# Optimization experiments

Hardware: AMD Instinct MI355X
Metric: run time of the kernel (lower is better)

The kernel has to match this reference:

```python
import jax, jax.numpy as jnp
import numpy as np

KH, KW = 3, 3

def setup_inputs() -> dict:
    key = jax.random.key(0)
    kx, kw = jax.random.split(key)
    X = jax.random.normal(kx, (4096, 8192), dtype=jnp.float32)
    # nn.Parameter(torch.rand(kernel_size)) -> uniform [0,1)
    weight = jax.random.uniform(kw, (KH, KW), dtype=jnp.float32)
    bias = jnp.zeros((1,), dtype=jnp.float32)
    return {"X": X, "weight": weight, "bias": bias}

def reference(X, weight, bias):
    # valid 2D cross-correlation (lax conv does correlation, no kernel flip)
    # X: [H, W]; weight: [kh, kw] -> out: [H-kh+1, W-kw+1]
    out = jax.lax.conv_general_dilated(
        X[None, None, :, :],            # NCHW, N=C=1
        weight[None, None, :, :],        # OIHW, O=I=1
        window_strides=(1, 1),
        padding="VALID",
    )[0, 0]
    return out + bias
```

## Files before the change

### kernel.cpp

```cpp
#include <hip/hip_runtime.h>

#define H  4096
#define W  8192
#define KH 3
#define KW 3
#define HO (H - KH + 1)
#define WO (W - KW + 1)
#define CPT 4
#define RPS 4
#define SPB 4
#define BAND (RPS * SPB)
#define BLK 256

__global__ __launch_bounds__(BLK) void ConvLayer_4140348473931_kernel(
    const float* __restrict__ X, const float* __restrict__ Wt,
    const float* __restrict__ Bias, float* __restrict__ Out)
{
    const int tid   = threadIdx.x;
    const int c0    = blockIdx.x * (BLK * CPT) + tid * CPT;
    const int rbase = blockIdx.y * BAND;
    const int cext  = min(c0 + 4, W - 2);

    float w[9];
#pragma unroll
    for (int i = 0; i < 9; ++i) w[i] = Wt[i];
    const float bias = Bias[0];

    float x[RPS + 2][6];
    float pre[RPS][6];

#define LOADROW(rr, dst)                                                     \
    do {                                                                     \
        int _r = (rr); if (_r > H - 1) _r = H - 1;                           \
        const float* _row = X + (size_t)_r * W;                              \
        float4 _v  = *reinterpret_cast<const float4*>(_row + c0);            \
        float2 _v2 = *reinterpret_cast<const float2*>(_row + cext);         \
        (dst)[0] = _v.x;  (dst)[1] = _v.y;  (dst)[2] = _v.z;                 \
        (dst)[3] = _v.w;  (dst)[4] = _v2.x; (dst)[5] = _v2.y;               \
    } while (0)

#pragma unroll
    for (int ir = 0; ir < 6; ++ir) LOADROW(rbase + ir, x[ir]);

#pragma unroll
    for (int s = 0; s < SPB; ++s) {
        if (s < SPB - 1) {
#pragma unroll
            for (int ir = 0; ir < RPS; ++ir)
                LOADROW(rbase + s * RPS + 6 + ir, pre[ir]);
        }

        float acc[RPS][CPT];
#pragma unroll
        for (int i = 0; i < RPS; ++i) {
#pragma unroll
            for (int j = 0; j < CPT; ++j) {
                float ss = bias;
#pragma unroll
                for (int kh = 0; kh < KH; ++kh)
#pragma unroll
                    for (int kw = 0; kw < KW; ++kw)
                        ss = fmaf(w[kh * 3 + kw], x[i + kh][j + kw], ss);
                acc[i][j] = ss;
            }
        }

        {
            const int r0 = rbase + s * RPS;
            const bool full = (c0 + CPT <= WO);
#pragma unroll
            for (int i = 0; i < RPS; ++i) {
                int r = r0 + i;
                if (r < HO) {
                    float* orow = Out + (size_t)r * WO + c0;
                    *reinterpret_cast<float2*>(orow) = make_float2(acc[i][0], acc[i][1]);
                    if (full)
                        *reinterpret_cast<float2*>(orow + 2) = make_float2(acc[i][2], acc[i][3]);
                }
            }
        }

        if (s < SPB - 1) {
#pragma unroll
            for (int j = 0; j < 6; ++j) { x[0][j] = x[4][j]; x[1][j] = x[5][j]; }
#pragma unroll
            for (int ir = 0; ir < RPS; ++ir)
#pragma unroll
                for (int j = 0; j < 6; ++j) x[2 + ir][j] = pre[ir][j];
        }
    }
#undef LOADROW
}

extern "C" void kernel_launch(void* const* d_in, const int* in_sizes, int n_in,
                              void* d_out, int out_size, void* d_ws, size_t ws_size,
                              hipStream_t stream) {
    const float* X    = (const float*)d_in[0];
    const float* Wt   = (const float*)d_in[1];
    const float* Bias = (const float*)d_in[2];
    float* Out        = (float*)d_out;

    dim3 block(BLK);
    dim3 grid((WO + BLK * CPT - 1) / (BLK * CPT),
              (HO + BAND - 1) / BAND);
    ConvLayer_4140348473931_kernel<<<grid, block, 0, stream>>>(X, Wt, Bias, Out);
}
```

Baseline: 48.87 us.

## Double-buffer row prefetch two stages ahead and double band height

Swaps the single prefetch buffer for two alternating buffers so that loads for stage s+2 are issued while stage s is computed and stored. The band per block grows from 16 to 32 rows, which halves the redundant halo-row reads, and launch bounds now request 4 blocks per SM. The goal is more memory-level parallelism in a bandwidth-bound stencil. In exchange it uses more registers and launches half as many blocks, which lowers parallelism.

```diff
diff --git a/kernel.cpp b/kernel.cpp
--- a/kernel.cpp
+++ b/kernel.cpp
@@ -8,11 +8,11 @@
 #define WO (W - KW + 1)
 #define CPT 4
 #define RPS 4
-#define SPB 4
+#define SPB 8
 #define BAND (RPS * SPB)
 #define BLK 256
 
-__global__ __launch_bounds__(BLK) void ConvLayer_4140348473931_kernel(
+__global__ __launch_bounds__(BLK, 4) void ConvLayer_4140348473931_kernel(
     const float* __restrict__ X, const float* __restrict__ Wt,
     const float* __restrict__ Bias, float* __restrict__ Out)
 {
@@ -26,70 +26,89 @@
     for (int i = 0; i < 9; ++i) w[i] = Wt[i];
     const float bias = Bias[0];
 
-    float x[RPS + 2][6];
-    float pre[RPS][6];
+    float x[6][6];
+    float preA[4][6];
+    float preB[4][6];
 
 #define LOADROW(rr, dst)                                                     \
     do {                                                                     \
         int _r = (rr); if (_r > H - 1) _r = H - 1;                           \
         const float* _row = X + (size_t)_r * W;                              \
         float4 _v  = *reinterpret_cast<const float4*>(_row + c0);            \
-        float2 _v2 = *reinterpret_cast<const float2*>(_row + cext);         \
+        float2 _v2 = *reinterpret_cast<const float2*>(_row + cext);          \
         (dst)[0] = _v.x;  (dst)[1] = _v.y;  (dst)[2] = _v.z;                 \
-        (dst)[3] = _v.w;  (dst)[4] = _v2.x; (dst)[5] = _v2.y;               \
+        (dst)[3] = _v.w;  (dst)[4] = _v2.x; (dst)[5] = _v2.y;                \
+    } while (0)
+
+#define PREFETCH(t, buf)                                                     \
+    do {                                                                     \
+        if ((t) < SPB) {                                                     \
+            _Pragma("unroll")                                                \
+            for (int _ir = 0; _ir < RPS; ++_ir)                              \
+                LOADROW(rbase + (t) * RPS + 2 + _ir, (buf)[_ir]);            \
+        }                                                                    \
+    } while (0)
+
+#define COMPUTE_STORE(s)                                                     \
+    do {                                                                     \
+        float acc[RPS][CPT];                                                 \
+        _Pragma("unroll")                                                    \
+        for (int _i = 0; _i < RPS; ++_i) {                                   \
+            _Pragma("unroll")                                                \
+            for (int _j = 0; _j < CPT; ++_j) {                               \
+                float _s = bias;                                             \
+                _Pragma("unroll")                                            \
+                for (int _kh = 0; _kh < KH; ++_kh)                           \
+                    _Pragma("unroll")                                        \
+                    for (int _kw = 0; _kw < KW; ++_kw)                       \
+                        _s = fmaf(w[_kh * 3 + _kw], x[_i + _kh][_j + _kw], _s); \
+                acc[_i][_j] = _s;                                            \
+            }                                                                \
+        }                                                                    \
+        const int _r0 = rbase + (s) * RPS;                                   \
+        const bool _full = (c0 + CPT <= WO);                                 \
+        _Pragma("unroll")                                                    \
+        for (int _i = 0; _i < RPS; ++_i) {                                   \
+            int _r = _r0 + _i;                                               \
+            if (_r < HO) {                                                   \
+                float* _orow = Out + (size_t)_r * WO + c0;                   \
+                *reinterpret_cast<float2*>(_orow) = make_float2(acc[_i][0], acc[_i][1]); \
+                if (_full)                                                   \
+                    *reinterpret_cast<float2*>(_orow + 2) = make_float2(acc[_i][2], acc[_i][3]); \
+            }                                                                \
+        }                                                                    \
+    } while (0)
+
+#define SHIFT_FROM(buf)                                                      \
+    do {                                                                     \
+        _Pragma("unroll")                                                    \
+        for (int _j = 0; _j < 6; ++_j) { x[0][_j] = x[4][_j]; x[1][_j] = x[5][_j]; } \
+        _Pragma("unroll")                                                    \
+        for (int _ir = 0; _ir < RPS; ++_ir)                                  \
+            _Pragma("unroll")                                                \
+            for (int _j = 0; _j < 6; ++_j) x[2 + _ir][_j] = (buf)[_ir][_j];  \
     } while (0)
 
 #pragma unroll
     for (int ir = 0; ir < 6; ++ir) LOADROW(rbase + ir, x[ir]);
+    PREFETCH(1, preA);
 
 #pragma unroll
-    for (int s = 0; s < SPB; ++s) {
-        if (s < SPB - 1) {
-#pragma unroll
-            for (int ir = 0; ir < RPS; ++ir)
-                LOADROW(rbase + s * RPS + 6 + ir, pre[ir]);
-        }
+    for (int p = 0; p < SPB / 2; ++p) {
+        const int s0 = 2 * p;
+        PREFETCH(s0 + 2, preB);
+        COMPUTE_STORE(s0);
+        SHIFT_FROM(preA);
 
-        float acc[RPS][CPT];
-#pragma unroll
-        for (int i = 0; i < RPS; ++i) {
-#pragma unroll
-            for (int j = 0; j < CPT; ++j) {
-                float ss = bias;
-#pragma unroll
-                for (int kh = 0; kh < KH; ++kh)
-#pragma unroll
-                    for (int kw = 0; kw < KW; ++kw)
-                        ss = fmaf(w[kh * 3 + kw], x[i + kh][j + kw], ss);
-                acc[i][j] = ss;
-            }
-        }
+        PREFETCH(s0 + 3, preA);
+        COMPUTE_STORE(s0 + 1);
+        if (s0 + 2 < SPB) SHIFT_FROM(preB);
+    }
 
-        {
-            const int r0 = rbase + s * RPS;
-            const bool full = (c0 + CPT <= WO);
-#pragma unroll
-            for (int i = 0; i < RPS; ++i) {
-                int r = r0 + i;
-                if (r < HO) {
-                    float* orow = Out + (size_t)r * WO + c0;
-                    *reinterpret_cast<float2*>(orow) = make_float2(acc[i][0], acc[i][1]);
-                    if (full)
-                        *reinterpret_cast<float2*>(orow + 2) = make_float2(acc[i][2], acc[i][3]);
-                }
-            }
-        }
-
-        if (s < SPB - 1) {
-#pragma unroll
-            for (int j = 0; j < 6; ++j) { x[0][j] = x[4][j]; x[1][j] = x[5][j]; }
-#pragma unroll
-            for (int ir = 0; ir < RPS; ++ir)
-#pragma unroll
-                for (int j = 0; j < 6; ++j) x[2 + ir][j] = pre[ir][j];
-        }
-    }
 #undef LOADROW
+#undef PREFETCH
+#undef COMPUTE_STORE
+#undef SHIFT_FROM
 }
 
 extern "C" void kernel_launch(void* const* d_in, const int* in_sizes, int n_in,
```

New measurement: 47.56 us (median of 2 runs). -2.7%, faster.

## Stage input tiles into LDS with async global_load_lds double buffering

Applied to the files above, without the earlier changes.

Replaces the per-thread register sliding-window loads with block tiles of 18x256 floats staged into shared memory through direct global-to-LDS loads, double buffered across 8 row tiles per block. Hand-placed vmcnt waits and barriers overlap the fetch of the next tile with the compute of the current one. The aim is to remove the redundant overlapping float2 halo loads and hide memory latency. In exchange it adds barriers, LDS traffic and halo recomputation, since each 256-wide tile yields only 252 output columns and 16-row tiles re-read 2 halo rows.

```diff
diff --git a/kernel.cpp b/kernel.cpp
--- a/kernel.cpp
+++ b/kernel.cpp
@@ -1,95 +1,127 @@
 #include <hip/hip_runtime.h>
 
-#define H  4096
-#define W  8192
-#define KH 3
-#define KW 3
-#define HO (H - KH + 1)
-#define WO (W - KW + 1)
-#define CPT 4
-#define RPS 4
-#define SPB 4
-#define BAND (RPS * SPB)
+#define H   4096
+#define W   8192
+#define HO  4094
+#define WO  8190
+#define TWI 256
+#define TWO 252
+#define TH  16
+#define IH  18
+#define TPB 8
 #define BLK 256
+
+typedef __attribute__((address_space(3))) void       lds_void;
+typedef __attribute__((address_space(1))) const void glob_void;
 
 __global__ __launch_bounds__(BLK) void ConvLayer_4140348473931_kernel(
     const float* __restrict__ X, const float* __restrict__ Wt,
     const float* __restrict__ Bias, float* __restrict__ Out)
 {
-    const int tid   = threadIdx.x;
-    const int c0    = blockIdx.x * (BLK * CPT) + tid * CPT;
-    const int rbase = blockIdx.y * BAND;
-    const int cext  = min(c0 + 4, W - 2);
+    __shared__ float bufA[IH][TWI];
+    __shared__ float bufB[IH][TWI];
+
+    const int tid  = threadIdx.x;
+    const int lane = tid & 63;
+    const int wav  = tid >> 6;
+
+    const int Cbase = blockIdx.x * TWO;
+    const int Rblk  = blockIdx.y * (TPB * TH);
+
+    const int gcol = min(Cbase + 4 * lane, W - 4);
 
     float w[9];
 #pragma unroll
     for (int i = 0; i < 9; ++i) w[i] = Wt[i];
     const float bias = Bias[0];
 
-    float x[RPS + 2][6];
-    float pre[RPS][6];
+    const int lr = wav * 4;
+    const int lc = lane * 4;
+    const int oc = Cbase + lc;
 
-#define LOADROW(rr, dst)                                                     \
-    do {                                                                     \
-        int _r = (rr); if (_r > H - 1) _r = H - 1;                           \
-        const float* _row = X + (size_t)_r * W;                              \
-        float4 _v  = *reinterpret_cast<const float4*>(_row + c0);            \
-        float2 _v2 = *reinterpret_cast<const float2*>(_row + cext);         \
-        (dst)[0] = _v.x;  (dst)[1] = _v.y;  (dst)[2] = _v.z;                 \
-        (dst)[3] = _v.w;  (dst)[4] = _v2.x; (dst)[5] = _v2.y;               \
+#define STAGE(BUF, R0)                                                        \
+    do {                                                                      \
+        _Pragma("unroll")                                                     \
+        for (int k = 0; k < 5; ++k) {                                         \
+            const int rr = wav + 4 * k;                                       \
+            if (rr < IH) {                                                    \
+                int gr = (R0) + rr; if (gr > H - 1) gr = H - 1;               \
+                const float* src = X + (size_t)gr * W + gcol;                 \
+                __builtin_amdgcn_global_load_lds(                             \
+                    (glob_void*)src, (lds_void*)&(BUF)[rr][0], 16, 0, 0);     \
+            }                                                                 \
+        }                                                                     \
     } while (0)
 
+#define WAITN()                                                               \
+    do { if (wav < 2) asm volatile("s_waitcnt vmcnt(5)" ::: "memory");        \
+         else         asm volatile("s_waitcnt vmcnt(4)" ::: "memory"); } while (0)
+#define WAIT0() asm volatile("s_waitcnt vmcnt(0)" ::: "memory")
+#define FENCE() asm volatile("" ::: "memory")
+#define BAR()   do { __builtin_amdgcn_s_barrier(); FENCE(); } while (0)
+
+#define CSTORE(BUF, R0)                                                       \
+    do {                                                                      \
+        float acc[4][4];                                                      \
+        _Pragma("unroll") for (int i = 0; i < 4; ++i)                         \
+        _Pragma("unroll") for (int j = 0; j < 4; ++j) acc[i][j] = bias;       \
+        _Pragma("unroll")                                                     \
+        for (int ir = 0; ir < 6; ++ir) {                                      \
+            float4 a4 = *reinterpret_cast<const float4*>(&(BUF)[lr + ir][lc]);\
+            float2 b2 = *reinterpret_cast<const float2*>(&(BUF)[lr + ir][lc + 4]); \
+            const float xw[6] = {a4.x, a4.y, a4.z, a4.w, b2.x, b2.y};         \
+            _Pragma("unroll")                                                 \
+            for (int i = 0; i < 4; ++i) {                                     \
+                const int kh = ir - i;                                        \
+                if (kh >= 0 && kh < 3) {                                      \
+                    _Pragma("unroll")                                         \
+                    for (int j = 0; j < 4; ++j) {                             \
+                        float s = acc[i][j];                                  \
+                        s = fmaf(w[kh * 3 + 0], xw[j + 0], s);                \
+                        s = fmaf(w[kh * 3 + 1], xw[j + 1], s);                \
+                        s = fmaf(w[kh * 3 + 2], xw[j + 2], s);                \
+                        acc[i][j] = s;                                        \
+                    }                                                         \
+                }                                                             \
+            }                                                                 \
+        }                                                                     \
+        if (lane < 63) {                                                      \
+            _Pragma("unroll")                                                 \
+            for (int i = 0; i < 4; ++i) {                                     \
+                const int r = (R0) + lr + i;                                  \
+                if (r < HO) {                                                 \
+                    float* orow = Out + (size_t)r * WO + oc;                  \
+                    if (oc + 2 <= WO)                                         \
+                        *reinterpret_cast<float2*>(orow) = make_float2(acc[i][0], acc[i][1]); \
+                    if (oc + 4 <= WO)                                         \
+                        *reinterpret_cast<float2*>(orow + 2) = make_float2(acc[i][2], acc[i][3]); \
+                }                                                             \
+            }                                                                 \
+        }                                                                     \
+    } while (0)
+
+    STAGE(bufA, Rblk);
 #pragma unroll
-    for (int ir = 0; ir < 6; ++ir) LOADROW(rbase + ir, x[ir]);
+    for (int t = 0; t < TPB; t += 2) {
+        const int R0 = Rblk + t * TH;
 
-#pragma unroll
-    for (int s = 0; s < SPB; ++s) {
-        if (s < SPB - 1) {
-#pragma unroll
-            for (int ir = 0; ir < RPS; ++ir)
-                LOADROW(rbase + s * RPS + 6 + ir, pre[ir]);
-        }
+        if (t + 1 < TPB) { STAGE(bufB, R0 + TH); WAITN(); } else { WAIT0(); }
+        BAR();
+        CSTORE(bufA, R0);
+        FENCE(); BAR();
 
-        float acc[RPS][CPT];
-#pragma unroll
-        for (int i = 0; i < RPS; ++i) {
-#pragma unroll
-            for (int j = 0; j < CPT; ++j) {
-                float ss = bias;
-#pragma unroll
-                for (int kh = 0; kh < KH; ++kh)
-#pragma unroll
-                    for (int kw = 0; kw < KW; ++kw)
-                        ss = fmaf(w[kh * 3 + kw], x[i + kh][j + kw], ss);
-                acc[i][j] = ss;
-            }
-        }
+        if (t + 2 < TPB) { STAGE(bufA, R0 + 2 * TH); WAITN(); } else { WAIT0(); }
+        BAR();
+        CSTORE(bufB, R0 + TH);
+        FENCE(); BAR();
+    }
 
-        {
-            const int r0 = rbase + s * RPS;
-            const bool full = (c0 + CPT <= WO);
-#pragma unroll
-            for (int i = 0; i < RPS; ++i) {
-                int r = r0 + i;
-                if (r < HO) {
-                    float* orow = Out + (size_t)r * WO + c0;
-                    *reinterpret_cast<float2*>(orow) = make_float2(acc[i][0], acc[i][1]);
-                    if (full)
-                        *reinterpret_cast<float2*>(orow + 2) = make_float2(acc[i][2], acc[i][3]);
-                }
-            }
-        }
-
-        if (s < SPB - 1) {
-#pragma unroll
-            for (int j = 0; j < 6; ++j) { x[0][j] = x[4][j]; x[1][j] = x[5][j]; }
-#pragma unroll
-            for (int ir = 0; ir < RPS; ++ir)
-#pragma unroll
-                for (int j = 0; j < 6; ++j) x[2 + ir][j] = pre[ir][j];
-        }
-    }
-#undef LOADROW
+#undef STAGE
+#undef WAITN
+#undef WAIT0
+#undef FENCE
+#undef BAR
+#undef CSTORE
 }
 
 extern "C" void kernel_launch(void* const* d_in, const int* in_sizes, int n_in,
@@ -101,7 +133,7 @@
     float* Out        = (float*)d_out;
 
     dim3 block(BLK);
-    dim3 grid((WO + BLK * CPT - 1) / (BLK * CPT),
-              (HO + BAND - 1) / BAND);
+    dim3 grid((WO + TWO - 1) / TWO,
+              (HO + TPB * TH - 1) / (TPB * TH));
     ConvLayer_4140348473931_kernel<<<grid, block, 0, stream>>>(X, Wt, Bias, Out);
 }
```

Result: slower. 53.07 us (+8.6%).
